# Performance work log

Hardware: AMD Instinct MI355X
Metric: run time of the kernel (lower is better)

## Reference

```python
import jax, jax.numpy as jnp
import numpy as np

N_NODES = 100000
N_EDGES = 1600000
IN_FEATS = 128
OUT_FEATS = 64


def setup_inputs() -> dict:
    key = jax.random.key(0)
    k1, k2, k3, k4 = jax.random.split(key, 4)
    feat = jax.random.normal(k1, (N_NODES, IN_FEATS), dtype=jnp.float32)
    # xavier-uniform-like init for weight
    limit = float(np.sqrt(6.0 / (IN_FEATS + OUT_FEATS)))
    weight = jax.random.uniform(k2, (IN_FEATS, OUT_FEATS), dtype=jnp.float32,
                                minval=-limit, maxval=limit)
    bias = jnp.zeros((OUT_FEATS,), dtype=jnp.float32)
    src = jax.random.randint(k3, (N_EDGES,), 0, N_NODES, dtype=jnp.int32)
    dst = jax.random.randint(k4, (N_EDGES,), 0, N_NODES, dtype=jnp.int32)
    return {"feat": feat, "weight": weight, "bias": bias, "src": src, "dst": dst}


def reference(feat, weight, bias, src, dst):
    # out-degree of each node (count of outgoing edges), clamped to >= 1
    ones = jnp.ones(src.shape[0], dtype=feat.dtype)
    degs = jax.ops.segment_sum(ones, src, num_segments=N_NODES)
    degs = jnp.clip(degs, 1.0, None)
    norm = degs ** -0.5  # [N]

    # dense linear then pre-aggregation degree scaling
    h = jnp.matmul(feat, weight) * norm[:, None]  # [N, out]

    # copy_src + sum aggregation: scatter-add messages h[src] into dst
    agg = jax.ops.segment_sum(h[src], dst, num_segments=N_NODES)  # [N, out]

    # post-aggregation degree scaling + bias (activation is None)
    rst = agg * norm[:, None] + bias
    return rst
```

## Files before the change

kernel.cpp:

```cpp
#include <hip/hip_runtime.h>
#include <hip/hip_bf16.h>

#define N_IN 128
#define N_OUT 64
#define BSHIFT 7
#define BNODES 128
#define MAXB 1024
#define CAP 4096
#define CH 4096

typedef short bf16x8 __attribute__((ext_vector_type(8)));
typedef float f32x4 __attribute__((ext_vector_type(4)));

__device__ inline short f2bf(float x) {
    __hip_bfloat16 b = __float2bfloat16(x);
    union { __hip_bfloat16 b; short s; } u;
    u.b = b;
    return u.s;
}

__device__ inline float bflo(unsigned int v) { return __uint_as_float(v << 16); }
__device__ inline float bfhi(unsigned int v) { return __uint_as_float(v & 0xffff0000u); }

__global__ __launch_bounds__(1024) void initcur_kernel(int* __restrict__ cursorS,
                                                       int* __restrict__ cursorD) {
    int i = threadIdx.x;
    cursorS[i] = i * CAP;
    cursorD[i] = i * CAP;
}

__global__ __launch_bounds__(512) void fillSB_kernel(const int* __restrict__ src,
                                                     const int* __restrict__ dst,
                                                     int* __restrict__ cursorS,
                                                     int* __restrict__ cursorD,
                                                     unsigned int* __restrict__ bufS,
                                                     unsigned int* __restrict__ bufD,
                                                     int nE, int nB) {
    __shared__ int hS[MAXB];
    __shared__ int hD[MAXB];
    __shared__ int lbS[MAXB];
    __shared__ int lbD[MAXB];
    int t = threadIdx.x;
    for (int i = t; i < nB; i += 512) { hS[i] = 0; hD[i] = 0; }
    __syncthreads();

    int e0 = blockIdx.x * 8192 + t;
    int sv[16], dv[16];
#pragma unroll
    for (int j = 0; j < 16; ++j) {
        int e = e0 + j * 512;
        if (e < nE) {
            sv[j] = src[e];
            dv[j] = dst[e];
            atomicAdd(&hS[sv[j] >> BSHIFT], 1);
            atomicAdd(&hD[dv[j] >> BSHIFT], 1);
        } else {
            sv[j] = -1;
            dv[j] = 0;
        }
    }
    __syncthreads();
    for (int i = t; i < nB; i += 512) {
        int c = hS[i];
        lbS[i] = c ? atomicAdd(&cursorS[i], c) : 0;
        c = hD[i];
        lbD[i] = c ? atomicAdd(&cursorD[i], c) : 0;
    }
    __syncthreads();
#pragma unroll
    for (int j = 0; j < 16; ++j) {
        if (sv[j] >= 0) {
            int ps = atomicAdd(&lbS[sv[j] >> BSHIFT], 1);
            bufS[ps] = (unsigned int)sv[j];
            int pd = atomicAdd(&lbD[dv[j] >> BSHIFT], 1);
            bufD[pd] = ((unsigned int)sv[j] << BSHIFT) | (unsigned int)(dv[j] & (BNODES - 1));
        }
    }
}

__global__ __launch_bounds__(256) void countS_kernel(const unsigned int* __restrict__ buf,
                                                     const int* __restrict__ cursorS,
                                                     float* __restrict__ nrm, int nN) {
    __shared__ int hist[BNODES];
    int t = threadIdx.x;
    if (t < BNODES) hist[t] = 0;
    __syncthreads();
    int b = blockIdx.x;
    int s = b * CAP, e = cursorS[b];
    for (int i = s + t; i < e; i += 256)
        atomicAdd(&hist[buf[i] & (BNODES - 1)], 1);
    __syncthreads();
    int node = b * BNODES + t;
    if (t < BNODES && node < nN)
        nrm[node] = rsqrtf(fmaxf((float)hist[t], 1.0f));
}

__global__ __launch_bounds__(256) void gemm_kernel(const float* __restrict__ feat,
                                                   const float* __restrict__ w,
                                                   const float* __restrict__ nrm,
                                                   __hip_bfloat16* __restrict__ h, int nN) {
    __shared__ short wt[N_OUT][N_IN + 8];
    int t = threadIdx.x;
    for (int i = t; i < N_IN * N_OUT; i += 256) {
        int k = i >> 6, c = i & 63;
        wt[c][k] = f2bf(w[i]);
    }
    __syncthreads();

    int wv = t >> 6, l = t & 63;
    int c16 = l & 15;
    int kq  = l >> 4;
    int nodeBase = blockIdx.x * 64 + wv * 16;
    int rowA = nodeBase + c16;
    int rowAc = min(rowA, nN - 1);

    f32x4 acc[4];
#pragma unroll
    for (int ct = 0; ct < 4; ++ct) acc[ct] = (f32x4){0.f, 0.f, 0.f, 0.f};

    const float* fptr = feat + (size_t)rowAc * N_IN + kq * 8;
#pragma unroll
    for (int ks = 0; ks < 4; ++ks) {
        float4 a0 = *(const float4*)(fptr + ks * 32);
        float4 a1 = *(const float4*)(fptr + ks * 32 + 4);
        union { bf16x8 v; short s[8]; } af;
        af.s[0] = f2bf(a0.x); af.s[1] = f2bf(a0.y);
        af.s[2] = f2bf(a0.z); af.s[3] = f2bf(a0.w);
        af.s[4] = f2bf(a1.x); af.s[5] = f2bf(a1.y);
        af.s[6] = f2bf(a1.z); af.s[7] = f2bf(a1.w);
#pragma unroll
        for (int ct = 0; ct < 4; ++ct) {
            bf16x8 bf = *(const bf16x8*)&wt[ct * 16 + c16][ks * 32 + kq * 8];
            acc[ct] = __builtin_amdgcn_mfma_f32_16x16x32_bf16(af.v, bf, acc[ct], 0, 0, 0);
        }
    }

#pragma unroll
    for (int r = 0; r < 4; ++r) {
        int node = nodeBase + 4 * kq + r;
        if (node < nN) {
            float nn = nrm[node];
#pragma unroll
            for (int ct = 0; ct < 4; ++ct) {
                short v = f2bf(acc[ct][r] * nn);
                *(short*)&h[(size_t)node * N_OUT + ct * 16 + c16] = v;
            }
        }
    }
}

__global__ __launch_bounds__(512) void agg_kernel(const unsigned int* __restrict__ buf,
                                                  const int* __restrict__ cursor,
                                                  const __hip_bfloat16* __restrict__ h,
                                                  const float* __restrict__ nrm,
                                                  const float* __restrict__ bias,
                                                  float* __restrict__ out, int nN) {
    __shared__ unsigned int sorted[CH];
    __shared__ int hist[BNODES];
    __shared__ int ssh[BNODES];
    __shared__ int sbase[BNODES];
    __shared__ int scur[BNODES];
    int t = threadIdx.x;
    int lane = t & 63, wv = t >> 6;
    int g = lane >> 4;
    int li = lane & 15;

    int b = blockIdx.x;
    int start = b * CAP;
    int end = cursor[b];

    float4 acc[4];
#pragma unroll
    for (int r = 0; r < 4; ++r) acc[r] = (float4){0.f, 0.f, 0.f, 0.f};

    for (int c0 = start; c0 < end; c0 += CH) {
        int cnt = min(end - c0, CH);
        for (int i = t; i < BNODES; i += 512) hist[i] = 0;
        __syncthreads();

        unsigned int pk[CH / 512];
#pragma unroll
        for (int j = 0; j < CH / 512; ++j) {
            int e = t + j * 512;
            if (e < cnt) {
                pk[j] = buf[c0 + e];
                atomicAdd(&hist[pk[j] & (BNODES - 1)], 1);
            } else {
                pk[j] = 0xFFFFFFFFu;
            }
        }
        __syncthreads();

        if (t < BNODES) ssh[t] = hist[t];
        __syncthreads();
        for (int o = 1; o < BNODES; o <<= 1) {
            int x = 0;
            if (t < BNODES && t >= o) x = ssh[t - o];
            __syncthreads();
            if (t < BNODES) ssh[t] += x;
            __syncthreads();
        }
        if (t < BNODES) {
            int ex = (t == 0) ? 0 : ssh[t - 1];
            sbase[t] = ex;
            scur[t] = ex;
        }
        __syncthreads();

#pragma unroll
        for (int j = 0; j < CH / 512; ++j) {
            if (pk[j] != 0xFFFFFFFFu) {
                int pos = atomicAdd(&scur[pk[j] & (BNODES - 1)], 1);
                sorted[pos] = pk[j];
            }
        }
        __syncthreads();

#pragma unroll
        for (int r = 0; r < 4; ++r) {
            int row = wv * 16 + r * 4 + g;
            int e = sbase[row], ee = scur[row];
            float4 a = acc[r];
            for (; e + 3 < ee; e += 4) {
                unsigned int p0 = sorted[e];
                unsigned int p1 = sorted[e + 1];
                unsigned int p2 = sorted[e + 2];
                unsigned int p3 = sorted[e + 3];
                uint2 v0 = *(const uint2*)&h[(size_t)(p0 >> BSHIFT) * N_OUT + li * 4];
                uint2 v1 = *(const uint2*)&h[(size_t)(p1 >> BSHIFT) * N_OUT + li * 4];
                uint2 v2 = *(const uint2*)&h[(size_t)(p2 >> BSHIFT) * N_OUT + li * 4];
                uint2 v3 = *(const uint2*)&h[(size_t)(p3 >> BSHIFT) * N_OUT + li * 4];
                a.x += bflo(v0.x); a.y += bfhi(v0.x); a.z += bflo(v0.y); a.w += bfhi(v0.y);
                a.x += bflo(v1.x); a.y += bfhi(v1.x); a.z += bflo(v1.y); a.w += bfhi(v1.y);
                a.x += bflo(v2.x); a.y += bfhi(v2.x); a.z += bflo(v2.y); a.w += bfhi(v2.y);
                a.x += bflo(v3.x); a.y += bfhi(v3.x); a.z += bflo(v3.y); a.w += bfhi(v3.y);
            }
            for (; e < ee; ++e) {
                unsigned int p = sorted[e];
                uint2 v = *(const uint2*)&h[(size_t)(p >> BSHIFT) * N_OUT + li * 4];
                a.x += bflo(v.x); a.y += bfhi(v.x); a.z += bflo(v.y); a.w += bfhi(v.y);
            }
            acc[r] = a;
        }
        __syncthreads();
    }

    float4 bl = ((const float4*)bias)[li];
    int nodeB = b * BNODES + wv * 16;
#pragma unroll
    for (int r = 0; r < 4; ++r) {
        int node = nodeB + r * 4 + g;
        if (node < nN) {
            float nn = nrm[node];
            float4 o4;
            o4.x = acc[r].x * nn + bl.x;
            o4.y = acc[r].y * nn + bl.y;
            o4.z = acc[r].z * nn + bl.z;
            o4.w = acc[r].w * nn + bl.w;
            *(float4*)&out[(size_t)node * N_OUT + li * 4] = o4;
        }
    }
}

extern "C" void kernel_launch(void* const* d_in, const int* in_sizes, int n_in,
                              void* d_out, int out_size, void* d_ws, size_t ws_size,
                              hipStream_t stream) {
    const float* feat = (const float*)d_in[0];
    const float* w    = (const float*)d_in[1];
    const float* bias = (const float*)d_in[2];
    const int*   src  = (const int*)d_in[3];
    const int*   dst  = (const int*)d_in[4];
    float* out = (float*)d_out;

    int nN = in_sizes[0] / N_IN;
    int nE = in_sizes[3];
    int nB = (nN + BNODES - 1) >> BSHIFT;

    size_t o = 0;
    auto alloc = [&](size_t bytes) { size_t r = o; o = (o + bytes + 1023) & ~(size_t)1023; return r; };
    char* wsc = (char*)d_ws;
    float* nrm    = (float*)(wsc + alloc((size_t)nN * 4));
    int* cursorS  = (int*)(wsc + alloc((size_t)MAXB * 4));
    int* cursor   = (int*)(wsc + alloc((size_t)MAXB * 4));
    unsigned int* bufD = (unsigned int*)(wsc + alloc((size_t)nB * CAP * 4));
    unsigned int* bufS = (unsigned int*)(wsc + alloc((size_t)nB * CAP * 4));
    __hip_bfloat16* h  = (__hip_bfloat16*)(wsc + alloc((size_t)nN * N_OUT * 2));

    int nblk = (nE + 8191) / 8192;
    initcur_kernel<<<1, 1024, 0, stream>>>(cursorS, cursor);
    fillSB_kernel<<<nblk, 512, 0, stream>>>(src, dst, cursorS, cursor, bufS, bufD, nE, nB);
    countS_kernel<<<nB, 256, 0, stream>>>(bufS, cursorS, nrm, nN);
    gemm_kernel<<<(nN + 63) / 64, 256, 0, stream>>>(feat, w, nrm, h, nN);
    agg_kernel<<<nB, 512, 0, stream>>>(bufD, cursor, h, nrm, bias, out, nN);
}
```

Before: 98.18 us.

## Split bucket cursors into 8 sub-slots and shrink fill blocks to spread atomics

Each destination and source bucket is split into 8 sub-regions of 512 entries, with one cursor per sub-region picked by block index modulo 8. This cuts contention on the global cursor atomics, and fill blocks now handle 2048 edges instead of 8192, so more blocks run. The source buffer stores only a byte (the local node index), which cuts countS traffic. The agg kernel first gathers the sub-regions into shared memory and does one sort pass with no chunk loop. If any bucket sub-slot gets more than 512 edges from its block group, it would overflow into the next sub-slot, so correctness depends on the degree distribution. LDS use also doubles.

```diff
diff --git a/kernel.cpp b/kernel.cpp
--- a/kernel.cpp
+++ b/kernel.cpp
@@ -7,7 +7,7 @@
 #define BNODES 128
 #define MAXB 1024
 #define CAP 4096
-#define CH 4096
+#define SUB 512
 
 typedef short bf16x8 __attribute__((ext_vector_type(8)));
 typedef float f32x4 __attribute__((ext_vector_type(4)));
@@ -24,16 +24,20 @@
 
 __global__ __launch_bounds__(1024) void initcur_kernel(int* __restrict__ cursorS,
                                                        int* __restrict__ cursorD) {
-    int i = threadIdx.x;
-    cursorS[i] = i * CAP;
-    cursorD[i] = i * CAP;
+    for (int i = threadIdx.x; i < 8 * MAXB; i += 1024) {
+        int x = i >> 10;
+        int b = i & (MAXB - 1);
+        int v = b * CAP + x * SUB;
+        cursorS[i] = v;
+        cursorD[i] = v;
+    }
 }
 
 __global__ __launch_bounds__(512) void fillSB_kernel(const int* __restrict__ src,
                                                      const int* __restrict__ dst,
                                                      int* __restrict__ cursorS,
                                                      int* __restrict__ cursorD,
-                                                     unsigned int* __restrict__ bufS,
+                                                     unsigned char* __restrict__ bufS,
                                                      unsigned int* __restrict__ bufD,
                                                      int nE, int nB) {
     __shared__ int hS[MAXB];
@@ -44,10 +48,14 @@
     for (int i = t; i < nB; i += 512) { hS[i] = 0; hD[i] = 0; }
     __syncthreads();
 
-    int e0 = blockIdx.x * 8192 + t;
-    int sv[16], dv[16];
-#pragma unroll
-    for (int j = 0; j < 16; ++j) {
+    int xg = blockIdx.x & 7;
+    int* curS = cursorS + xg * MAXB;
+    int* curD = cursorD + xg * MAXB;
+
+    int e0 = blockIdx.x * 2048 + t;
+    int sv[4], dv[4];
+#pragma unroll
+    for (int j = 0; j < 4; ++j) {
         int e = e0 + j * 512;
         if (e < nE) {
             sv[j] = src[e];
@@ -62,23 +70,23 @@
     __syncthreads();
     for (int i = t; i < nB; i += 512) {
         int c = hS[i];
-        lbS[i] = c ? atomicAdd(&cursorS[i], c) : 0;
+        lbS[i] = c ? atomicAdd(&curS[i], c) : 0;
         c = hD[i];
-        lbD[i] = c ? atomicAdd(&cursorD[i], c) : 0;
-    }
-    __syncthreads();
-#pragma unroll
-    for (int j = 0; j < 16; ++j) {
+        lbD[i] = c ? atomicAdd(&curD[i], c) : 0;
+    }
+    __syncthreads();
+#pragma unroll
+    for (int j = 0; j < 4; ++j) {
         if (sv[j] >= 0) {
             int ps = atomicAdd(&lbS[sv[j] >> BSHIFT], 1);
-            bufS[ps] = (unsigned int)sv[j];
+            bufS[ps] = (unsigned char)(sv[j] & (BNODES - 1));
             int pd = atomicAdd(&lbD[dv[j] >> BSHIFT], 1);
             bufD[pd] = ((unsigned int)sv[j] << BSHIFT) | (unsigned int)(dv[j] & (BNODES - 1));
         }
     }
 }
 
-__global__ __launch_bounds__(256) void countS_kernel(const unsigned int* __restrict__ buf,
+__global__ __launch_bounds__(256) void countS_kernel(const unsigned char* __restrict__ bufS,
                                                      const int* __restrict__ cursorS,
                                                      float* __restrict__ nrm, int nN) {
     __shared__ int hist[BNODES];
@@ -86,9 +94,13 @@
     if (t < BNODES) hist[t] = 0;
     __syncthreads();
     int b = blockIdx.x;
-    int s = b * CAP, e = cursorS[b];
-    for (int i = s + t; i < e; i += 256)
-        atomicAdd(&hist[buf[i] & (BNODES - 1)], 1);
+#pragma unroll
+    for (int x = 0; x < 8; ++x) {
+        int s0 = b * CAP + x * SUB;
+        int len = cursorS[x * MAXB + b] - s0;
+        for (int i = t; i < len; i += 256)
+            atomicAdd(&hist[bufS[s0 + i] & (BNODES - 1)], 1);
+    }
     __syncthreads();
     int node = b * BNODES + t;
     if (t < BNODES && node < nN)
@@ -149,13 +161,14 @@
     }
 }
 
-__global__ __launch_bounds__(512) void agg_kernel(const unsigned int* __restrict__ buf,
-                                                  const int* __restrict__ cursor,
+__global__ __launch_bounds__(512) void agg_kernel(const unsigned int* __restrict__ bufD,
+                                                  const int* __restrict__ cursorD,
                                                   const __hip_bfloat16* __restrict__ h,
                                                   const float* __restrict__ nrm,
                                                   const float* __restrict__ bias,
                                                   float* __restrict__ out, int nN) {
-    __shared__ unsigned int sorted[CH];
+    __shared__ unsigned int stage[CAP];
+    __shared__ unsigned int sorted_[CAP];
     __shared__ int hist[BNODES];
     __shared__ int ssh[BNODES];
     __shared__ int sbase[BNODES];
@@ -166,83 +179,87 @@
     int li = lane & 15;
 
     int b = blockIdx.x;
-    int start = b * CAP;
-    int end = cursor[b];
+
+    int off = 0;
+#pragma unroll
+    for (int x = 0; x < 8; ++x) {
+        int s0 = b * CAP + x * SUB;
+        int len = cursorD[x * MAXB + b] - s0;
+        for (int i = t; i < len; i += 512) stage[off + i] = bufD[s0 + i];
+        off += len;
+    }
+    int cnt = off;
+
+    for (int i = t; i < BNODES; i += 512) hist[i] = 0;
+    __syncthreads();
+
+    unsigned int pk[CAP / 512];
+#pragma unroll
+    for (int j = 0; j < CAP / 512; ++j) {
+        int e = t + j * 512;
+        if (e < cnt) {
+            pk[j] = stage[e];
+            atomicAdd(&hist[pk[j] & (BNODES - 1)], 1);
+        } else {
+            pk[j] = 0xFFFFFFFFu;
+        }
+    }
+    __syncthreads();
+
+    if (t < BNODES) ssh[t] = hist[t];
+    __syncthreads();
+    for (int o = 1; o < BNODES; o <<= 1) {
+        int x = 0;
+        if (t < BNODES && t >= o) x = ssh[t - o];
+        __syncthreads();
+        if (t < BNODES) ssh[t] += x;
+        __syncthreads();
+    }
+    if (t < BNODES) {
+        int ex = (t == 0) ? 0 : ssh[t - 1];
+        sbase[t] = ex;
+        scur[t] = ex;
+    }
+    __syncthreads();
+
+#pragma unroll
+    for (int j = 0; j < CAP / 512; ++j) {
+        if (pk[j] != 0xFFFFFFFFu) {
+            int pos = atomicAdd(&scur[pk[j] & (BNODES - 1)], 1);
+            sorted_[pos] = pk[j];
+        }
+    }
+    __syncthreads();
 
     float4 acc[4];
 #pragma unroll
     for (int r = 0; r < 4; ++r) acc[r] = (float4){0.f, 0.f, 0.f, 0.f};
 
-    for (int c0 = start; c0 < end; c0 += CH) {
-        int cnt = min(end - c0, CH);
-        for (int i = t; i < BNODES; i += 512) hist[i] = 0;
-        __syncthreads();
-
-        unsigned int pk[CH / 512];
-#pragma unroll
-        for (int j = 0; j < CH / 512; ++j) {
-            int e = t + j * 512;
-            if (e < cnt) {
-                pk[j] = buf[c0 + e];
-                atomicAdd(&hist[pk[j] & (BNODES - 1)], 1);
-            } else {
-                pk[j] = 0xFFFFFFFFu;
-            }
-        }
-        __syncthreads();
-
-        if (t < BNODES) ssh[t] = hist[t];
-        __syncthreads();
-        for (int o = 1; o < BNODES; o <<= 1) {
-            int x = 0;
-            if (t < BNODES && t >= o) x = ssh[t - o];
-            __syncthreads();
-            if (t < BNODES) ssh[t] += x;
-            __syncthreads();
-        }
-        if (t < BNODES) {
-            int ex = (t == 0) ? 0 : ssh[t - 1];
-            sbase[t] = ex;
-            scur[t] = ex;
-        }
-        __syncthreads();
-
-#pragma unroll
-        for (int j = 0; j < CH / 512; ++j) {
-            if (pk[j] != 0xFFFFFFFFu) {
-                int pos = atomicAdd(&scur[pk[j] & (BNODES - 1)], 1);
-                sorted[pos] = pk[j];
-            }
-        }
-        __syncthreads();
-
-#pragma unroll
-        for (int r = 0; r < 4; ++r) {
-            int row = wv * 16 + r * 4 + g;
-            int e = sbase[row], ee = scur[row];
-            float4 a = acc[r];
-            for (; e + 3 < ee; e += 4) {
-                unsigned int p0 = sorted[e];
-                unsigned int p1 = sorted[e + 1];
-                unsigned int p2 = sorted[e + 2];
-                unsigned int p3 = sorted[e + 3];
-                uint2 v0 = *(const uint2*)&h[(size_t)(p0 >> BSHIFT) * N_OUT + li * 4];
-                uint2 v1 = *(const uint2*)&h[(size_t)(p1 >> BSHIFT) * N_OUT + li * 4];
-                uint2 v2 = *(const uint2*)&h[(size_t)(p2 >> BSHIFT) * N_OUT + li * 4];
-                uint2 v3 = *(const uint2*)&h[(size_t)(p3 >> BSHIFT) * N_OUT + li * 4];
-                a.x += bflo(v0.x); a.y += bfhi(v0.x); a.z += bflo(v0.y); a.w += bfhi(v0.y);
-                a.x += bflo(v1.x); a.y += bfhi(v1.x); a.z += bflo(v1.y); a.w += bfhi(v1.y);
-                a.x += bflo(v2.x); a.y += bfhi(v2.x); a.z += bflo(v2.y); a.w += bfhi(v2.y);
-                a.x += bflo(v3.x); a.y += bfhi(v3.x); a.z += bflo(v3.y); a.w += bfhi(v3.y);
-            }
-            for (; e < ee; ++e) {
-                unsigned int p = sorted[e];
-                uint2 v = *(const uint2*)&h[(size_t)(p >> BSHIFT) * N_OUT + li * 4];
-                a.x += bflo(v.x); a.y += bfhi(v.x); a.z += bflo(v.y); a.w += bfhi(v.y);
-            }
-            acc[r] = a;
-        }
-        __syncthreads();
+#pragma unroll
+    for (int r = 0; r < 4; ++r) {
+        int row = wv * 16 + r * 4 + g;
+        int e = sbase[row], ee = scur[row];
+        float4 a = acc[r];
+        for (; e + 3 < ee; e += 4) {
+            unsigned int p0 = sorted_[e];
+            unsigned int p1 = sorted_[e + 1];
+            unsigned int p2 = sorted_[e + 2];
+            unsigned int p3 = sorted_[e + 3];
+            uint2 v0 = *(const uint2*)&h[(size_t)(p0 >> BSHIFT) * N_OUT + li * 4];
+            uint2 v1 = *(const uint2*)&h[(size_t)(p1 >> BSHIFT) * N_OUT + li * 4];
+            uint2 v2 = *(const uint2*)&h[(size_t)(p2 >> BSHIFT) * N_OUT + li * 4];
+            uint2 v3 = *(const uint2*)&h[(size_t)(p3 >> BSHIFT) * N_OUT + li * 4];
+            a.x += bflo(v0.x); a.y += bfhi(v0.x); a.z += bflo(v0.y); a.w += bfhi(v0.y);
+            a.x += bflo(v1.x); a.y += bfhi(v1.x); a.z += bflo(v1.y); a.w += bfhi(v1.y);
+            a.x += bflo(v2.x); a.y += bfhi(v2.x); a.z += bflo(v2.y); a.w += bfhi(v2.y);
+            a.x += bflo(v3.x); a.y += bfhi(v3.x); a.z += bflo(v3.y); a.w += bfhi(v3.y);
+        }
+        for (; e < ee; ++e) {
+            unsigned int p = sorted_[e];
+            uint2 v = *(const uint2*)&h[(size_t)(p >> BSHIFT) * N_OUT + li * 4];
+            a.x += bflo(v.x); a.y += bfhi(v.x); a.z += bflo(v.y); a.w += bfhi(v.y);
+        }
+        acc[r] = a;
     }
 
     float4 bl = ((const float4*)bias)[li];
@@ -280,16 +297,16 @@
     auto alloc = [&](size_t bytes) { size_t r = o; o = (o + bytes + 1023) & ~(size_t)1023; return r; };
     char* wsc = (char*)d_ws;
     float* nrm    = (float*)(wsc + alloc((size_t)nN * 4));
-    int* cursorS  = (int*)(wsc + alloc((size_t)MAXB * 4));
-    int* cursor   = (int*)(wsc + alloc((size_t)MAXB * 4));
-    unsigned int* bufD = (unsigned int*)(wsc + alloc((size_t)nB * CAP * 4));
-    unsigned int* bufS = (unsigned int*)(wsc + alloc((size_t)nB * CAP * 4));
-    __hip_bfloat16* h  = (__hip_bfloat16*)(wsc + alloc((size_t)nN * N_OUT * 2));
-
-    int nblk = (nE + 8191) / 8192;
-    initcur_kernel<<<1, 1024, 0, stream>>>(cursorS, cursor);
-    fillSB_kernel<<<nblk, 512, 0, stream>>>(src, dst, cursorS, cursor, bufS, bufD, nE, nB);
+    int* cursorS  = (int*)(wsc + alloc((size_t)(8 * MAXB) * 4));
+    int* cursorD  = (int*)(wsc + alloc((size_t)(8 * MAXB) * 4));
+    unsigned int* bufD  = (unsigned int*)(wsc + alloc((size_t)nB * CAP * 4));
+    unsigned char* bufS = (unsigned char*)(wsc + alloc((size_t)nB * CAP));
+    __hip_bfloat16* h   = (__hip_bfloat16*)(wsc + alloc((size_t)nN * N_OUT * 2));
+
+    int nblk = (nE + 2047) / 2048;
+    initcur_kernel<<<1, 1024, 0, stream>>>(cursorS, cursorD);
+    fillSB_kernel<<<nblk, 512, 0, stream>>>(src, dst, cursorS, cursorD, bufS, bufD, nE, nB);
     countS_kernel<<<nB, 256, 0, stream>>>(bufS, cursorS, nrm, nN);
     gemm_kernel<<<(nN + 63) / 64, 256, 0, stream>>>(feat, w, nrm, h, nN);
-    agg_kernel<<<nB, 512, 0, stream>>>(bufD, cursor, h, nrm, bias, out, nN);
-}
+    agg_kernel<<<nB, 512, 0, stream>>>(bufD, cursorD, h, nrm, bias, out, nN);
+}
```

After: 97.75 us. About the same (-0.4%).
